# Kernel tuning notes

Measured on AMD Instinct MI355X. Metric: run time of the kernel, lower is better.

## Reference

```python
import jax, jax.numpy as jnp
import numpy as np

N_NODES = 50000
DEG = 32
HEADS = 4
OUT_F = 16
IN_F = 64
NEG_SLOPE = 0.01  # jax.nn.leaky_relu default


def setup_inputs() -> dict:
    key = jax.random.key(0)
    k_adj, k_mask, k_q, k_qw, k_kw, k_aw = jax.random.split(key, 6)
    adj = jax.random.randint(k_adj, (N_NODES, DEG), 0, N_NODES)
    pad = jax.random.uniform(k_mask, (N_NODES, DEG)) < 0.1
    adj = jnp.where(pad, -1, adj)
    Q = jax.random.normal(k_q, (IN_F, N_NODES), dtype=jnp.float32)
    qw_scale = 2 * np.sqrt(6.0 / (IN_F + OUT_F * HEADS))
    kw_scale = qw_scale
    a_scale = 2 * np.sqrt(6.0 / (OUT_F + HEADS))
    query_weight = (jax.random.uniform(k_qw, (HEADS, OUT_F, IN_F)) - 0.5) * qw_scale
    key_weight = (jax.random.uniform(k_kw, (HEADS, OUT_F, IN_F)) - 0.5) * kw_scale
    attn_weight = (jax.random.uniform(k_aw, (HEADS, OUT_F)) - 0.5) * a_scale
    return {
        'adj': adj,
        'Q': Q,
        'query_weight': query_weight.astype(jnp.float32),
        'key_weight': key_weight.astype(jnp.float32),
        'attn_weight': attn_weight.astype(jnp.float32),
    }


def reference(adj, Q, query_weight, key_weight, attn_weight):
    # K defaults to Q (self-attention over graph)
    K = Q
    # project keys: [H, O, N], then gather neighbors -> [H, O, N, deg]
    Ko = jnp.einsum('hoi,in->hon', key_weight, K)[..., adj]
    # project queries: [H, O, N]
    Qo = jnp.einsum('hoi,in->hon', query_weight, Q)
    # per-edge pre-activation and attention logits
    X = jax.nn.leaky_relu(Qo[..., None] + Ko, negative_slope=NEG_SLOPE)
    X = jnp.einsum('honk,ho->hnk', X, attn_weight)  # [H, N, deg]
    X = jnp.where(adj == -1, -jnp.inf, X)
    # rows with zero valid neighbors -> zero logits (uniform softmax, masked later)
    X = jnp.where((adj != -1).sum(-1, keepdims=True) == 0, 0.0, X)
    attn = jax.nn.softmax(X, axis=-1)
    # weighted aggregate of gathered keys -> [H, O, N]
    return jnp.einsum('hnk,honk->hon', jnp.where(adj == -1, 0.0, attn), Ko)
```

## Files before the change

### kernel.cpp

```cpp
#include <hip/hip_runtime.h>
#include <math.h>

#define DEG 32
#define NHO 64
#define NPW 4
#define NPB 16

typedef short  frag8  __attribute__((ext_vector_type(8)));
typedef float  f32x4  __attribute__((ext_vector_type(4)));

template <int CTRL>
__device__ __forceinline__ float dpp_add(float v) {
    int t = __builtin_amdgcn_update_dpp(0, __float_as_int(v), CTRL, 0xF, 0xF, true);
    return v + __int_as_float(t);
}

__device__ __forceinline__ unsigned bf16_rne(float f) {
    unsigned u = __float_as_uint(f);
    return (u + 0x7fffu + ((u >> 16) & 1u)) >> 16;
}

__global__ __launch_bounds__(256) void proj_mfma_kernel(
    const float* __restrict__ Q,
    const float* __restrict__ Wq,
    const float* __restrict__ Wk,
    float* __restrict__ Pq,
    unsigned short* __restrict__ Pkb,
    int N)
{
    __shared__ unsigned qlds[64 * 33];
    __shared__ unsigned wlds[128 * 33];

    int t  = threadIdx.x;
    int n0 = blockIdx.x * 64;

    {
        int l    = t >> 1;
        int half = t & 1;
        const float* wr = (l < 64 ? Wq + (size_t)l * 64
                                  : Wk + (size_t)(l - 64) * 64) + half * 32;
#pragma unroll
        for (int r = 0; r < 16; r++) {
            float f0 = wr[2 * r], f1 = wr[2 * r + 1];
            wlds[l * 33 + half * 16 + r] = bf16_rne(f0) | (bf16_rne(f1) << 16);
        }
    }
    {
        int n  = t & 63;
        int gn = n0 + n;
        bool act = (gn < N);
#pragma unroll
        for (int r = 0; r < 8; r++) {
            int dp = (t >> 6) * 8 + r;
            int k  = dp * 2;
            float f0 = act ? Q[(size_t)k * N + gn] : 0.f;
            float f1 = act ? Q[(size_t)(k + 1) * N + gn] : 0.f;
            qlds[n * 33 + dp] = bf16_rne(f0) | (bf16_rne(f1) << 16);
        }
    }
    __syncthreads();

    int lane = t & 63;
    int w    = t >> 6;
    int li   = lane & 15;
    int quad = lane >> 4;

    f32x4 acc[8];
#pragma unroll
    for (int ot = 0; ot < 8; ot++) acc[ot] = (f32x4){0.f, 0.f, 0.f, 0.f};

#pragma unroll
    for (int ks = 0; ks < 2; ks++) {
        union { unsigned u[4]; frag8 f; } A;
        int abase = (w * 16 + li) * 33 + ks * 16 + quad * 4;
#pragma unroll
        for (int c = 0; c < 4; c++) A.u[c] = qlds[abase + c];
#pragma unroll
        for (int ot = 0; ot < 8; ot++) {
            union { unsigned u[4]; frag8 f; } B;
            int bbase = (ot * 16 + li) * 33 + ks * 16 + quad * 4;
#pragma unroll
            for (int c = 0; c < 4; c++) B.u[c] = wlds[bbase + c];
            acc[ot] = __builtin_amdgcn_mfma_f32_16x16x32_bf16(A.f, B.f, acc[ot],
                                                              0, 0, 0);
        }
    }

#pragma unroll
    for (int ot = 0; ot < 8; ot++) {
#pragma unroll
        for (int r = 0; r < 4; r++) {
            int node = n0 + w * 16 + quad * 4 + r;
            if (node < N) {
                float v = acc[ot][r];
                if (ot < 4) {
                    Pq[(size_t)node * NHO + ot * 16 + li] = v;
                } else {
                    Pkb[(size_t)node * NHO + (ot - 4) * 16 + li] =
                        (unsigned short)bf16_rne(v);
                }
            }
        }
    }
}

__global__ __launch_bounds__(256) void gat_kernel(
    const int*            __restrict__ adj,
    const float*          __restrict__ Pq,
    const unsigned short* __restrict__ Pkb,
    const float*          __restrict__ aw,
    float*                __restrict__ out,
    int N)
{
    __shared__ float tile[NHO][NPB + 1];

    int lane = threadIdx.x & 63;
    int wv   = threadIdx.x >> 6;

    float a2l = aw[lane] * 1.44269504f;
    float c1  = 0.505f * a2l;
    float c2  = 0.495f * a2l;

    int nbase = blockIdx.x * NPB + wv * NPW;

#pragma unroll 1
    for (int ni = 0; ni < NPW; ni++) {
        int n = nbase + ni;
        float r = 0.f;
        if (n < N) {
            float qv  = Pq[(size_t)n * NHO + lane];
            int jreg  = (lane < DEG) ? adj[(size_t)n * DEG + lane] : -1;
            float c1q = c1 * qv;

            unsigned short raw[DEG];
            int jv[DEG];
#pragma unroll
            for (int t = 0; t < DEG; t++) {
                int j = __builtin_amdgcn_readlane(jreg, t);
                jv[t] = j;
                const unsigned short* row =
                    Pkb + (((size_t)(j < 0 ? 0 : j)) << 6);
                raw[t] = row[lane];
            }

            float s = 0.f, acc = 0.f;
#pragma unroll
            for (int t = 0; t < DEG; t++) {
                float kv = __uint_as_float((unsigned)raw[t] << 16);
                float x  = qv + kv;
                float tt = fmaf(c1, kv, c1q);
                float c  = fmaf(c2, fabsf(x), tt);
                c = dpp_add<0xB1>(c);
                c = dpp_add<0x4E>(c);
                c = dpp_add<0x141>(c);
                c = dpp_add<0x140>(c);
                float lg = (jv[t] >= 0) ? c : -1e30f;
                float p  = __builtin_amdgcn_exp2f(lg);
                s   += p;
                acc  = fmaf(p, kv, acc);
            }
            r = (s > 0.f) ? acc * __builtin_amdgcn_rcpf(s) : 0.f;
        }
        tile[lane][wv * NPW + ni] = r;
    }
    __syncthreads();

    int n0 = blockIdx.x * NPB;
    int l  = threadIdx.x >> 2;
    int c4 = threadIdx.x & 3;
    int nc = n0 + c4 * 4;
    float4 v = make_float4(tile[l][c4 * 4 + 0], tile[l][c4 * 4 + 1],
                           tile[l][c4 * 4 + 2], tile[l][c4 * 4 + 3]);
    if (nc + 3 < N) {
        *(float4*)(out + (size_t)l * N + nc) = v;
    } else {
#pragma unroll
        for (int e = 0; e < 4; e++)
            if (nc + e < N) out[(size_t)l * N + nc + e] = (&v.x)[e];
    }
}

extern "C" void kernel_launch(void* const* d_in, const int* in_sizes, int n_in,
                              void* d_out, int out_size, void* d_ws, size_t ws_size,
                              hipStream_t stream) {
    const int*   adj = (const int*)  d_in[0];
    const float* Q   = (const float*)d_in[1];
    const float* qw  = (const float*)d_in[2];
    const float* kw  = (const float*)d_in[3];
    const float* aw  = (const float*)d_in[4];
    float*       out = (float*)d_out;

    int N = in_sizes[0] / DEG;

    float*          Pq  = (float*)d_ws;
    unsigned short* Pkb = (unsigned short*)(Pq + (size_t)N * NHO);

    proj_mfma_kernel<<<(N + 63) / 64, 256, 0, stream>>>(Q, qw, kw, Pq, Pkb, N);

    gat_kernel<<<(N + NPB - 1) / NPB, 256, 0, stream>>>(adj, Pq, Pkb, aw, out, N);
}
```

Baseline: 127.0 us.

## Split wave into two neighbor slots with two features per lane in GAT kernel

Each lane now handles two adjacent features via 32-bit packed bf16 loads. The two wave halves process different neighbors (16 each), using ds_bpermute to broadcast adjacency indices, and the halves' partial softmax sums are combined with a cross-half bpermute at the end. This halves the serial per-neighbor loop length and the number of gather instructions, at the cost of extra bpermute traffic and a 3-step DPP reduction over 16 lanes. It also relies on unnormalized exp2 without max subtraction, as before.

```diff
diff --git a/kernel.cpp b/kernel.cpp
--- a/kernel.cpp
+++ b/kernel.cpp
@@ -114,69 +114,88 @@
 {
     __shared__ float tile[NHO][NPB + 1];
 
-    int lane = threadIdx.x & 63;
+    int l    = threadIdx.x & 63;
     int wv   = threadIdx.x >> 6;
-
-    float a2l = aw[lane] * 1.44269504f;
-    float c1  = 0.505f * a2l;
-    float c2  = 0.495f * a2l;
+    int sl   = l & 31;
+    int slot = l >> 5;
+
+    const unsigned* Pk32 = (const unsigned*)Pkb;
+
+    float2 awp = *(const float2*)(aw + 2 * sl);
+    const float L2E = 1.44269504f;
+    float c1_0 = 0.505f * L2E * awp.x, c2_0 = 0.495f * L2E * awp.x;
+    float c1_1 = 0.505f * L2E * awp.y, c2_1 = 0.495f * L2E * awp.y;
+
+    int bprm_it0 = slot * 64;
+    int bprm_xor = (l ^ 32) * 4;
 
     int nbase = blockIdx.x * NPB + wv * NPW;
 
 #pragma unroll 1
     for (int ni = 0; ni < NPW; ni++) {
         int n = nbase + ni;
-        float r = 0.f;
         if (n < N) {
-            float qv  = Pq[(size_t)n * NHO + lane];
-            int jreg  = (lane < DEG) ? adj[(size_t)n * DEG + lane] : -1;
-            float c1q = c1 * qv;
-
-            unsigned short raw[DEG];
-            int jv[DEG];
-#pragma unroll
-            for (int t = 0; t < DEG; t++) {
-                int j = __builtin_amdgcn_readlane(jreg, t);
+            float2 qp = *(const float2*)(Pq + (size_t)n * NHO + 2 * sl);
+            int adjA  = adj[(size_t)n * DEG + sl];
+            float c1q = fmaf(c1_1, qp.y, c1_0 * qp.x);
+
+            int      jv[16];
+            unsigned kvr[16];
+#pragma unroll
+            for (int t = 0; t < 16; t++) {
+                int j = __builtin_amdgcn_ds_bpermute(bprm_it0 + t * 4, adjA);
                 jv[t] = j;
-                const unsigned short* row =
-                    Pkb + (((size_t)(j < 0 ? 0 : j)) << 6);
-                raw[t] = row[lane];
-            }
-
-            float s = 0.f, acc = 0.f;
-#pragma unroll
-            for (int t = 0; t < DEG; t++) {
-                float kv = __uint_as_float((unsigned)raw[t] << 16);
-                float x  = qv + kv;
-                float tt = fmaf(c1, kv, c1q);
-                float c  = fmaf(c2, fabsf(x), tt);
+                unsigned off = (((unsigned)(j < 0 ? 0 : j)) << 5) + sl;
+                kvr[t] = Pk32[off];
+            }
+
+            float s = 0.f, a0 = 0.f, a1 = 0.f;
+#pragma unroll
+            for (int t = 0; t < 16; t++) {
+                float kv0 = __uint_as_float(kvr[t] << 16);
+                float kv1 = __uint_as_float(kvr[t] & 0xffff0000u);
+                float x0  = qp.x + kv0;
+                float x1  = qp.y + kv1;
+                float c   = fmaf(c1_0, kv0, c1q);
+                c = fmaf(c1_1, kv1, c);
+                c = fmaf(c2_0, fabsf(x0), c);
+                c = fmaf(c2_1, fabsf(x1), c);
                 c = dpp_add<0xB1>(c);
                 c = dpp_add<0x4E>(c);
                 c = dpp_add<0x141>(c);
-                c = dpp_add<0x140>(c);
-                float lg = (jv[t] >= 0) ? c : -1e30f;
-                float p  = __builtin_amdgcn_exp2f(lg);
-                s   += p;
-                acc  = fmaf(p, kv, acc);
-            }
-            r = (s > 0.f) ? acc * __builtin_amdgcn_rcpf(s) : 0.f;
-        }
-        tile[lane][wv * NPW + ni] = r;
+                float p = __builtin_amdgcn_exp2f(c);
+                p = (jv[t] >= 0) ? p : 0.f;
+                s += p;
+                a0 = fmaf(p, kv0, a0);
+                a1 = fmaf(p, kv1, a1);
+            }
+
+            s  += __int_as_float(__builtin_amdgcn_ds_bpermute(bprm_xor, __float_as_int(s)));
+            a0 += __int_as_float(__builtin_amdgcn_ds_bpermute(bprm_xor, __float_as_int(a0)));
+            a1 += __int_as_float(__builtin_amdgcn_ds_bpermute(bprm_xor, __float_as_int(a1)));
+
+            float rs = (s > 0.f) ? __builtin_amdgcn_rcpf(s) : 0.f;
+            if (slot == 0) {
+                int col = wv * NPW + ni;
+                tile[2 * sl + 0][col] = a0 * rs;
+                tile[2 * sl + 1][col] = a1 * rs;
+            }
+        }
     }
     __syncthreads();
 
     int n0 = blockIdx.x * NPB;
-    int l  = threadIdx.x >> 2;
+    int lr = threadIdx.x >> 2;
     int c4 = threadIdx.x & 3;
     int nc = n0 + c4 * 4;
-    float4 v = make_float4(tile[l][c4 * 4 + 0], tile[l][c4 * 4 + 1],
-                           tile[l][c4 * 4 + 2], tile[l][c4 * 4 + 3]);
+    float4 v = make_float4(tile[lr][c4 * 4 + 0], tile[lr][c4 * 4 + 1],
+                           tile[lr][c4 * 4 + 2], tile[lr][c4 * 4 + 3]);
     if (nc + 3 < N) {
-        *(float4*)(out + (size_t)l * N + nc) = v;
+        *(float4*)(out + (size_t)lr * N + nc) = v;
     } else {
 #pragma unroll
         for (int e = 0; e < 4; e++)
-            if (nc + e < N) out[(size_t)l * N + nc + e] = (&v.x)[e];
+            if (nc + e < N) out[(size_t)lr * N + nc + e] = (&v.x)[e];
     }
 }
 
```

New measurement: 111.6 us. 12.1% less time.
